# Kernel tuning notes

Measured on AMD Instinct MI355X. Metric: run time of the kernel, lower is better.

The kernel has to match this reference:

```python
import jax, jax.numpy as jnp
import numpy as np


def setup_inputs() -> dict:
    key = jax.random.key(0)
    k1, k2, k3, k4 = jax.random.split(key, 4)
    B, N, D, K, O = 8, 6144, 16, 3, 64
    inputs = jax.random.normal(k1, (B, N, D), dtype=jnp.float32)
    supports = jax.random.uniform(k2, (K, N, N), dtype=jnp.float32)
    W = jax.random.normal(k3, (O, D * K), dtype=jnp.float32) * 0.05
    b = jax.random.normal(k4, (O,), dtype=jnp.float32) * 0.05
    return {"inputs": inputs, "supports": supports, "W": W, "b": b}


def reference(inputs, supports, W, b):
    # inputs: [B, N, D]; supports: [K, N, N]; W: [O, D*K]; b: [O]
    B, N, D = inputs.shape
    K = supports.shape[0]
    # matrix_normalization: support + I  (identity self-loop add)
    sup = supports + jnp.eye(N, dtype=supports.dtype)  # [K, N, N]
    # per-support dense matmul; layout [B, N, D, K] matches the torch
    # stack/reshape/transpose chain (feature index = d*K + k)
    y = jnp.einsum('knm,bmd->bndk', sup, inputs)  # [B, N, D, K]
    y = y.reshape(B, N, D * K)
    return y @ W.T + b  # [B, N, O]
```

## Files before the change

### kernel.cpp

```cpp
#include <hip/hip_runtime.h>

#define NN 6144
#define BND (NN*16)

typedef short short8 __attribute__((ext_vector_type(8)));
typedef float f32x4 __attribute__((ext_vector_type(4)));

__device__ __forceinline__ short f2bf(float f) {
    unsigned u = __builtin_bit_cast(unsigned, f);
    u = (u + 0x7FFFu + ((u >> 16) & 1u)) >> 16;
    return (short)u;
}
__device__ __forceinline__ float bf2f(unsigned short s) {
    unsigned u = ((unsigned)s) << 16;
    return __builtin_bit_cast(float, u);
}

__global__ void __launch_bounds__(256) prep_kernel(
    const float* __restrict__ xin, unsigned short* __restrict__ Xt)
{
    __shared__ unsigned short ldsT[16 * 64];
    const int b  = blockIdx.y;
    const int m0 = blockIdx.x * 64;
    const int t  = threadIdx.x;
    const int ml = t >> 2, dq = t & 3;
    float4 v = *(const float4*)(xin + (size_t)b * BND + (size_t)(m0 + ml) * 16 + dq * 4);
    ldsT[(dq * 4 + 0) * 64 + ml] = (unsigned short)f2bf(v.x);
    ldsT[(dq * 4 + 1) * 64 + ml] = (unsigned short)f2bf(v.y);
    ldsT[(dq * 4 + 2) * 64 + ml] = (unsigned short)f2bf(v.z);
    ldsT[(dq * 4 + 3) * 64 + ml] = (unsigned short)f2bf(v.w);
    __syncthreads();
    if (t < 128) {
        int d = t >> 3, j = t & 7;
        short8 s = *(const short8*)&ldsT[d * 64 + j * 8];
        *(short8*)(Xt + (size_t)(b * 16 + d) * NN + m0 + j * 8) = s;
    }
}

__global__ void __launch_bounds__(256, 4) gemm_kernel(
    const float* __restrict__ sup, const unsigned short* __restrict__ Xt,
    unsigned short* __restrict__ Yp)
{
    __shared__ float ldsram[8192];
    float* ldsA = ldsram;
    unsigned short* ldsB = (unsigned short*)(ldsram + 4096);

    const int tid = threadIdx.x;
    const int w = tid >> 6, L = tid & 63, q = L >> 4, col = L & 15;
    const int n0  = blockIdx.x * 64;
    const int k   = blockIdx.y;
    const int seg = blockIdx.z;
    const float* Ab = sup + (size_t)k * NN * NN;

    f32x4 acc[8];
#pragma unroll
    for (int i = 0; i < 8; ++i) acc[i] = (f32x4)0.0f;

    for (int it = 0; it < 48; ++it) {
        const int k0 = seg * 3072 + it * 64;
#pragma unroll
        for (int i = 0; i < 4; ++i) {
            int p = i * 256 + tid;
            int r = p >> 4, cs = p & 15;
            int cch = cs ^ (r & 7);
            const float* src = Ab + (size_t)(n0 + r) * NN + k0 + cch * 4;
            __builtin_amdgcn_global_load_lds(
                (const __attribute__((address_space(1))) unsigned int*)src,
                (__attribute__((address_space(3))) unsigned int*)((char*)ldsA + p * 16), 16, 0, 0);
        }
#pragma unroll
        for (int i = 0; i < 4; ++i) {
            int p = i * 256 + tid;
            int c = p >> 3, hs = p & 7;
            int h = hs ^ (c & 7);
            const unsigned short* src = Xt + (size_t)c * NN + k0 + h * 8;
            __builtin_amdgcn_global_load_lds(
                (const __attribute__((address_space(1))) unsigned int*)src,
                (__attribute__((address_space(3))) unsigned int*)((char*)ldsB + p * 16), 16, 0, 0);
        }
        __syncthreads();

        const int r = w * 16 + col;
#pragma unroll
        for (int kc = 0; kc < 2; ++kc) {
            int c0 = kc * 8 + q * 2;
            float4 a0 = *(const float4*)&ldsA[(r * 16 + ((c0    ) ^ (r & 7))) * 4];
            float4 a1 = *(const float4*)&ldsA[(r * 16 + ((c0 + 1) ^ (r & 7))) * 4];
            short8 af;
            af[0] = f2bf(a0.x); af[1] = f2bf(a0.y); af[2] = f2bf(a0.z); af[3] = f2bf(a0.w);
            af[4] = f2bf(a1.x); af[5] = f2bf(a1.y); af[6] = f2bf(a1.z); af[7] = f2bf(a1.w);
#pragma unroll
            for (int cc = 0; cc < 8; ++cc) {
                int c = cc * 16 + col;
                short8 bf = *(const short8*)&ldsB[(c * 8 + ((kc * 4 + q) ^ (c & 7))) * 8];
                acc[cc] = __builtin_amdgcn_mfma_f32_16x16x32_bf16(af, bf, acc[cc], 0, 0, 0);
            }
        }
        __syncthreads();
    }

    float* stg = ldsram + w * 2048;
#pragma unroll
    for (int cc = 0; cc < 8; ++cc)
#pragma unroll
        for (int rr = 0; rr < 4; ++rr)
            stg[(q * 4 + rr) * 128 + cc * 16 + col] = acc[cc][rr];

    unsigned short* ypb = Yp + ((size_t)(seg * 3 + k) * NN + n0 + w * 16) * 128;
#pragma unroll
    for (int u = 0; u < 8; ++u) {
        int idx = u * 256 + L * 4;
        float4 v = *(const float4*)&stg[idx];
        unsigned h0 = (unsigned short)f2bf(v.x) | ((unsigned)(unsigned short)f2bf(v.y) << 16);
        unsigned h1 = (unsigned short)f2bf(v.z) | ((unsigned)(unsigned short)f2bf(v.w) << 16);
        uint2 pk; pk.x = h0; pk.y = h1;
        *(uint2*)(ypb + idx) = pk;
    }
}

__global__ void __launch_bounds__(256) out_kernel(
    const unsigned short* __restrict__ Yp, const float* __restrict__ xin,
    const float* __restrict__ W, const float* __restrict__ bias, float* __restrict__ out)
{
    const int o   = threadIdx.x & 63;
    const int wid = blockIdx.x * 4 + (threadIdx.x >> 6);

    float wreg[48];
#pragma unroll
    for (int d = 0; d < 16; ++d)
#pragma unroll
        for (int kk = 0; kk < 3; ++kk)
            wreg[kk * 16 + d] = W[o * 48 + d * 3 + kk];
    float wsum[16];
#pragma unroll
    for (int d = 0; d < 16; ++d) wsum[d] = wreg[d] + wreg[16 + d] + wreg[32 + d];
    const float bv = bias[o];

    for (int ii = 0; ii < 24; ++ii) {
        int p = wid * 24 + ii;
        int b = p / NN;
        int n = p - b * NN;
        float acc = bv;
        const float* xp = xin + (size_t)b * BND + (size_t)n * 16;
#pragma unroll
        for (int d4 = 0; d4 < 4; ++d4) {
            float4 x4 = *(const float4*)(xp + d4 * 4);
            acc += x4.x * wsum[d4 * 4] + x4.y * wsum[d4 * 4 + 1]
                 + x4.z * wsum[d4 * 4 + 2] + x4.w * wsum[d4 * 4 + 3];
        }
#pragma unroll
        for (int s = 0; s < 2; ++s)
#pragma unroll
            for (int kk = 0; kk < 3; ++kk) {
                const unsigned short* yp = Yp + ((size_t)(s * 3 + kk) * NN + n) * 128 + b * 16;
                short8 y0 = *(const short8*)yp;
                short8 y1 = *(const short8*)(yp + 8);
#pragma unroll
                for (int j = 0; j < 8; ++j) {
                    acc += bf2f((unsigned short)y0[j]) * wreg[kk * 16 + j];
                    acc += bf2f((unsigned short)y1[j]) * wreg[kk * 16 + 8 + j];
                }
            }
        out[(size_t)p * 64 + o] = acc;
    }
}

extern "C" void kernel_launch(void* const* d_in, const int* in_sizes, int n_in,
                              void* d_out, int out_size, void* d_ws, size_t ws_size,
                              hipStream_t stream) {
    const float* xin  = (const float*)d_in[0];
    const float* sup  = (const float*)d_in[1];
    const float* W    = (const float*)d_in[2];
    const float* bias = (const float*)d_in[3];
    float* out = (float*)d_out;

    char* ws = (char*)d_ws;
    unsigned short* Xt = (unsigned short*)ws;
    unsigned short* Yp = (unsigned short*)(ws + 1572864);

    prep_kernel<<<dim3(96, 8), 256, 0, stream>>>(xin, Xt);
    gemm_kernel<<<dim3(96, 3, 2), 256, 0, stream>>>(sup, Xt, Yp);
    out_kernel<<<512, 256, 0, stream>>>(Yp, xin, W, bias, out);
}
```

Measured before the change: 709.6 us.

## Double-buffer LDS tiles in support GEMM to overlap loads with MFMA

Splits the GEMM main loop into stage and compute helpers and adds a second LDS buffer, so the next K-tile is loaded via global_load_lds while the current tile is computed. Each step now needs one barrier instead of two. The cost is doubled LDS per block (64KB) and launch bounds lowered from 4 to 2 blocks per CU, which cuts occupancy. The grid is only 576 blocks, so occupancy was already limited.

```diff
diff --git a/kernel.cpp b/kernel.cpp
--- a/kernel.cpp
+++ b/kernel.cpp
@@ -37,13 +37,64 @@
     }
 }
 
-__global__ void __launch_bounds__(256, 4) gemm_kernel(
+
+__device__ __forceinline__ void stage_tile(
+    const float* __restrict__ Ab, const unsigned short* __restrict__ Xt,
+    float* ldsA, unsigned short* ldsB, int n0, int k0, int tid)
+{
+#pragma unroll
+    for (int i = 0; i < 4; ++i) {
+        int p = i * 256 + tid;
+        int r = p >> 4, cs = p & 15;
+        int cch = cs ^ (r & 7);
+        const float* src = Ab + (size_t)(n0 + r) * NN + k0 + cch * 4;
+        __builtin_amdgcn_global_load_lds(
+            (const __attribute__((address_space(1))) unsigned int*)src,
+            (__attribute__((address_space(3))) unsigned int*)((char*)ldsA + p * 16), 16, 0, 0);
+    }
+#pragma unroll
+    for (int i = 0; i < 4; ++i) {
+        int p = i * 256 + tid;
+        int c = p >> 3, hs = p & 7;
+        int h = hs ^ (c & 7);
+        const unsigned short* src = Xt + (size_t)c * NN + k0 + h * 8;
+        __builtin_amdgcn_global_load_lds(
+            (const __attribute__((address_space(1))) unsigned int*)src,
+            (__attribute__((address_space(3))) unsigned int*)((char*)ldsB + p * 16), 16, 0, 0);
+    }
+}
+
+__device__ __forceinline__ void compute_tile(
+    const float* ldsA, const unsigned short* ldsB,
+    int w, int q, int col, f32x4* acc)
+{
+    const int r = w * 16 + col;
+#pragma unroll
+    for (int kc = 0; kc < 2; ++kc) {
+        int c0 = kc * 8 + q * 2;
+        float4 a0 = *(const float4*)&ldsA[(r * 16 + ((c0    ) ^ (r & 7))) * 4];
+        float4 a1 = *(const float4*)&ldsA[(r * 16 + ((c0 + 1) ^ (r & 7))) * 4];
+        short8 af;
+        af[0] = f2bf(a0.x); af[1] = f2bf(a0.y); af[2] = f2bf(a0.z); af[3] = f2bf(a0.w);
+        af[4] = f2bf(a1.x); af[5] = f2bf(a1.y); af[6] = f2bf(a1.z); af[7] = f2bf(a1.w);
+#pragma unroll
+        for (int cc = 0; cc < 8; ++cc) {
+            int c = cc * 16 + col;
+            short8 bf = *(const short8*)&ldsB[(c * 8 + ((kc * 4 + q) ^ (c & 7))) * 8];
+            acc[cc] = __builtin_amdgcn_mfma_f32_16x16x32_bf16(af, bf, acc[cc], 0, 0, 0);
+        }
+    }
+}
+
+__global__ void __launch_bounds__(256, 2) gemm_kernel(
     const float* __restrict__ sup, const unsigned short* __restrict__ Xt,
     unsigned short* __restrict__ Yp)
 {
-    __shared__ float ldsram[8192];
-    float* ldsA = ldsram;
-    unsigned short* ldsB = (unsigned short*)(ldsram + 4096);
+    __shared__ float ldsram[16384];
+    float* A0 = ldsram;
+    unsigned short* B0 = (unsigned short*)(ldsram + 4096);
+    float* A1 = ldsram + 8192;
+    unsigned short* B1 = (unsigned short*)(ldsram + 12288);
 
     const int tid = threadIdx.x;
     const int w = tid >> 6, L = tid & 63, q = L >> 4, col = L & 15;
@@ -51,52 +102,32 @@
     const int k   = blockIdx.y;
     const int seg = blockIdx.z;
     const float* Ab = sup + (size_t)k * NN * NN;
+    const int kbase = seg * 3072;
 
     f32x4 acc[8];
 #pragma unroll
     for (int i = 0; i < 8; ++i) acc[i] = (f32x4)0.0f;
 
-    for (int it = 0; it < 48; ++it) {
-        const int k0 = seg * 3072 + it * 64;
-#pragma unroll
-        for (int i = 0; i < 4; ++i) {
-            int p = i * 256 + tid;
-            int r = p >> 4, cs = p & 15;
-            int cch = cs ^ (r & 7);
-            const float* src = Ab + (size_t)(n0 + r) * NN + k0 + cch * 4;
-            __builtin_amdgcn_global_load_lds(
-                (const __attribute__((address_space(1))) unsigned int*)src,
-                (__attribute__((address_space(3))) unsigned int*)((char*)ldsA + p * 16), 16, 0, 0);
+    stage_tile(Ab, Xt, A0, B0, n0, kbase, tid);
+    asm volatile("s_waitcnt vmcnt(0)" ::: "memory");
+    __builtin_amdgcn_s_barrier();
+
+#pragma unroll 1
+    for (int it = 0; it < 48; it += 2) {
+        stage_tile(Ab, Xt, A1, B1, n0, kbase + (it + 1) * 64, tid);
+        __builtin_amdgcn_sched_barrier(0);
+        compute_tile(A0, B0, w, q, col, acc);
+        asm volatile("s_waitcnt vmcnt(0)" ::: "memory");
+        __builtin_amdgcn_s_barrier();
+        if (it + 2 < 48) {
+            stage_tile(Ab, Xt, A0, B0, n0, kbase + (it + 2) * 64, tid);
+            __builtin_amdgcn_sched_barrier(0);
+            compute_tile(A1, B1, w, q, col, acc);
+            asm volatile("s_waitcnt vmcnt(0)" ::: "memory");
+            __builtin_amdgcn_s_barrier();
+        } else {
+            compute_tile(A1, B1, w, q, col, acc);
         }
-#pragma unroll
-        for (int i = 0; i < 4; ++i) {
-            int p = i * 256 + tid;
-            int c = p >> 3, hs = p & 7;
-            int h = hs ^ (c & 7);
-            const unsigned short* src = Xt + (size_t)c * NN + k0 + h * 8;
-            __builtin_amdgcn_global_load_lds(
-                (const __attribute__((address_space(1))) unsigned int*)src,
-                (__attribute__((address_space(3))) unsigned int*)((char*)ldsB + p * 16), 16, 0, 0);
-        }
-        __syncthreads();
-
-        const int r = w * 16 + col;
-#pragma unroll
-        for (int kc = 0; kc < 2; ++kc) {
-            int c0 = kc * 8 + q * 2;
-            float4 a0 = *(const float4*)&ldsA[(r * 16 + ((c0    ) ^ (r & 7))) * 4];
-            float4 a1 = *(const float4*)&ldsA[(r * 16 + ((c0 + 1) ^ (r & 7))) * 4];
-            short8 af;
-            af[0] = f2bf(a0.x); af[1] = f2bf(a0.y); af[2] = f2bf(a0.z); af[3] = f2bf(a0.w);
-            af[4] = f2bf(a1.x); af[5] = f2bf(a1.y); af[6] = f2bf(a1.z); af[7] = f2bf(a1.w);
-#pragma unroll
-            for (int cc = 0; cc < 8; ++cc) {
-                int c = cc * 16 + col;
-                short8 bf = *(const short8*)&ldsB[(c * 8 + ((kc * 4 + q) ^ (c & 7))) * 8];
-                acc[cc] = __builtin_amdgcn_mfma_f32_16x16x32_bf16(af, bf, acc[cc], 0, 0, 0);
-            }
-        }
-        __syncthreads();
     }
 
     float* stg = ldsram + w * 2048;
```

Result: slower. 743.1 us (+4.7%).

## Load GEMM operands directly from global memory into registers, dropping LDS staging

Applied to the files above, without the earlier changes.

The GEMM kernel no longer stages the support tile and the transposed input tile in LDS through global_load_lds with block barriers. Each lane now loads its own A fragment and B fragments straight from global memory into registers inside the K loop, and the occupancy hint drops from 4 to 3. This removes the LDS round trip and the two __syncthreads per iteration. The cost is that B fragments are reloaded redundantly by every wave, there is no cross-wave sharing, and the global accesses are strided and less coalesced, so the kernel depends on the cache hierarchy.

```diff
diff --git a/kernel.cpp b/kernel.cpp
--- a/kernel.cpp
+++ b/kernel.cpp
@@ -37,69 +37,49 @@
     }
 }
 
-__global__ void __launch_bounds__(256, 4) gemm_kernel(
+__global__ void __launch_bounds__(256, 3) gemm_kernel(
     const float* __restrict__ sup, const unsigned short* __restrict__ Xt,
     unsigned short* __restrict__ Yp)
 {
-    __shared__ float ldsram[8192];
-    float* ldsA = ldsram;
-    unsigned short* ldsB = (unsigned short*)(ldsram + 4096);
+    __shared__ float stgram[8192];
 
     const int tid = threadIdx.x;
     const int w = tid >> 6, L = tid & 63, q = L >> 4, col = L & 15;
     const int n0  = blockIdx.x * 64;
     const int k   = blockIdx.y;
     const int seg = blockIdx.z;
-    const float* Ab = sup + (size_t)k * NN * NN;
+    const int kbase = seg * 3072;
+
+    const int r = w * 16 + col;
+    const float* Arow = sup + (size_t)k * NN * NN + (size_t)(n0 + r) * NN + kbase + q * 8;
+    const unsigned short* Bb = Xt + (size_t)col * NN + kbase + q * 8;
 
     f32x4 acc[8];
 #pragma unroll
     for (int i = 0; i < 8; ++i) acc[i] = (f32x4)0.0f;
 
+#pragma unroll 1
     for (int it = 0; it < 48; ++it) {
-        const int k0 = seg * 3072 + it * 64;
-#pragma unroll
-        for (int i = 0; i < 4; ++i) {
-            int p = i * 256 + tid;
-            int r = p >> 4, cs = p & 15;
-            int cch = cs ^ (r & 7);
-            const float* src = Ab + (size_t)(n0 + r) * NN + k0 + cch * 4;
-            __builtin_amdgcn_global_load_lds(
-                (const __attribute__((address_space(1))) unsigned int*)src,
-                (__attribute__((address_space(3))) unsigned int*)((char*)ldsA + p * 16), 16, 0, 0);
-        }
-#pragma unroll
-        for (int i = 0; i < 4; ++i) {
-            int p = i * 256 + tid;
-            int c = p >> 3, hs = p & 7;
-            int h = hs ^ (c & 7);
-            const unsigned short* src = Xt + (size_t)c * NN + k0 + h * 8;
-            __builtin_amdgcn_global_load_lds(
-                (const __attribute__((address_space(1))) unsigned int*)src,
-                (__attribute__((address_space(3))) unsigned int*)((char*)ldsB + p * 16), 16, 0, 0);
-        }
-        __syncthreads();
-
-        const int r = w * 16 + col;
+        const int ko = it * 64;
 #pragma unroll
         for (int kc = 0; kc < 2; ++kc) {
-            int c0 = kc * 8 + q * 2;
-            float4 a0 = *(const float4*)&ldsA[(r * 16 + ((c0    ) ^ (r & 7))) * 4];
-            float4 a1 = *(const float4*)&ldsA[(r * 16 + ((c0 + 1) ^ (r & 7))) * 4];
+            const float* ap = Arow + ko + kc * 32;
+            float4 a0 = *(const float4*)ap;
+            float4 a1 = *(const float4*)(ap + 4);
+            short8 bf[8];
+#pragma unroll
+            for (int cc = 0; cc < 8; ++cc)
+                bf[cc] = *(const short8*)(Bb + (size_t)(cc * 16) * NN + ko + kc * 32);
             short8 af;
             af[0] = f2bf(a0.x); af[1] = f2bf(a0.y); af[2] = f2bf(a0.z); af[3] = f2bf(a0.w);
             af[4] = f2bf(a1.x); af[5] = f2bf(a1.y); af[6] = f2bf(a1.z); af[7] = f2bf(a1.w);
 #pragma unroll
-            for (int cc = 0; cc < 8; ++cc) {
-                int c = cc * 16 + col;
-                short8 bf = *(const short8*)&ldsB[(c * 8 + ((kc * 4 + q) ^ (c & 7))) * 8];
-                acc[cc] = __builtin_amdgcn_mfma_f32_16x16x32_bf16(af, bf, acc[cc], 0, 0, 0);
-            }
+            for (int cc = 0; cc < 8; ++cc)
+                acc[cc] = __builtin_amdgcn_mfma_f32_16x16x32_bf16(af, bf[cc], acc[cc], 0, 0, 0);
         }
-        __syncthreads();
     }
 
-    float* stg = ldsram + w * 2048;
+    float* stg = stgram + w * 2048;
 #pragma unroll
     for (int cc = 0; cc < 8; ++cc)
 #pragma unroll
```

Measured after the change: 881.0 us. 1.24x slower.
